# Kernel tuning notes

Hardware: AMD Instinct MI355X
Metric: run time of the kernel (lower is better)

## Reference

```python
import jax, jax.numpy as jnp
import numpy as np

N = 50000   # nodes
E = 800000  # edges (avg degree 16)
IN, HID, OUT = 128, 128, 64


def setup_inputs() -> dict:
    key = jax.random.key(0)
    ks = jax.random.split(key, 8)
    x = jax.random.normal(ks[0], (N, IN), dtype=jnp.float32)
    edge_index = jax.random.randint(ks[1], (2, E), 0, N, dtype=jnp.int32)
    s = 0.05
    W1 = jax.random.normal(ks[2], (IN, HID), dtype=jnp.float32) * s
    b1 = jnp.zeros((HID,), dtype=jnp.float32)
    W2 = jax.random.normal(ks[3], (HID, HID), dtype=jnp.float32) * s
    b2 = jnp.zeros((HID,), dtype=jnp.float32)
    W3 = jax.random.normal(ks[4], (HID, OUT), dtype=jnp.float32) * s
    b3 = jnp.zeros((OUT,), dtype=jnp.float32)
    return {"x": x, "edge_index": edge_index, "W1": W1, "b1": b1,
            "W2": W2, "b2": b2, "W3": W3, "b3": b3}


def _gcn_norm(edge_index, n):
    # PyG GCNConv default: add self-loops, symmetric normalization D^-1/2 A D^-1/2
    loop = jnp.arange(n, dtype=edge_index.dtype)
    src = jnp.concatenate([edge_index[0], loop])  # [E+N]
    dst = jnp.concatenate([edge_index[1], loop])  # [E+N]
    deg = jax.ops.segment_sum(jnp.ones_like(dst, dtype=jnp.float32), dst,
                              num_segments=n)  # degree of destination (col)
    dinv = jax.lax.rsqrt(deg)  # deg >= 1 due to self-loops
    norm = dinv[src] * dinv[dst]  # [E+N]
    return src, dst, norm


def _gcn_conv(x, src, dst, norm, W, b, n):
    h = x @ W                      # [N, F_out]  (transform first, fewer flops)
    msg = h[src] * norm[:, None]   # gather + scale  [E+N, F_out]
    agg = jax.ops.segment_sum(msg, dst, num_segments=n)
    return agg + b


def reference(x, edge_index, W1, b1, W2, b2, W3, b3):
    n = x.shape[0]
    src, dst, norm = _gcn_norm(edge_index, n)
    h = jax.nn.relu(_gcn_conv(x, src, dst, norm, W1, b1, n))
    h = jax.nn.relu(_gcn_conv(h, src, dst, norm, W2, b2, n))
    # dropout p=0.0 / eval mode -> identity
    out = jax.nn.relu(h @ W3 + b3)
    return out
```

## Files before the change

### kernel.cpp

```cpp
#include <hip/hip_runtime.h>
#include <hip/hip_fp16.h>
#include <cstddef>
#include <type_traits>


typedef _Float16 half8 __attribute__((ext_vector_type(8)));
typedef float f32x4 __attribute__((ext_vector_type(4)));

constexpr int CAP = 4608;

__global__ __launch_bounds__(256) void prep(const float* __restrict__ x,
                                            __half* __restrict__ xh, int n4, int ncast,
                                            const float* __restrict__ W1,
                                            const float* __restrict__ W2,
                                            const float* __restrict__ W3,
                                            __half* __restrict__ w1t,
                                            __half* __restrict__ w2t,
                                            __half* __restrict__ w3t,
                                            int* __restrict__ gcount, int nb) {
    int b = blockIdx.x;
    if (b == 0 && threadIdx.x < nb) gcount[threadIdx.x] = 0;
    if (b < ncast) {
        int i = b * 256 + threadIdx.x;
        if (i < n4) {
            float4 v = *(const float4*)&x[(size_t)i * 4];
            __half2 a = __floats2half2_rn(v.x, v.y);
            __half2 c = __floats2half2_rn(v.z, v.w);
            *(int2*)&xh[(size_t)i * 4] = make_int2(*(int*)&a, *(int*)&c);
        }
        return;
    }
    int blk = b - ncast;
    const float* W;
    __half* Wt;
    int ncol, i;
    if (blk < 64) { W = W1; Wt = w1t; ncol = 128; i = blk * 256 + threadIdx.x; }
    else if (blk < 128) { W = W2; Wt = w2t; ncol = 128; i = (blk - 64) * 256 + threadIdx.x; }
    else { W = W3; Wt = w3t; ncol = 64; i = (blk - 128) * 256 + threadIdx.x; }
    if (i < 128 * ncol) {
        int k = i / ncol, c = i - k * ncol;
        Wt[c * 128 + k] = __float2half(W[i]);
    }
}

__global__ __launch_bounds__(1024) void bucket_p1(const int* __restrict__ src,
                                                  const int* __restrict__ dst,
                                                  int* __restrict__ gcount,
                                                  int2* __restrict__ gbucket,
                                                  int nb, int e) {
    __shared__ int lcnt[256];
    __shared__ int lbase[256];
    int t = threadIdx.x;
    if (t < nb) lcnt[t] = 0;
    __syncthreads();

    int base = blockIdx.x * 8192 + t * 8;
    int d[8], s[8], pb[8], pp[8];
    if (base + 8 <= e) {
        *(int4*)&d[0] = *(const int4*)&dst[base];
        *(int4*)&d[4] = *(const int4*)&dst[base + 4];
        *(int4*)&s[0] = *(const int4*)&src[base];
        *(int4*)&s[4] = *(const int4*)&src[base + 4];
    } else {
#pragma unroll
        for (int u = 0; u < 8; ++u) {
            d[u] = (base + u < e) ? dst[base + u] : -1;
            s[u] = (base + u < e) ? src[base + u] : 0;
        }
    }
#pragma unroll
    for (int u = 0; u < 8; ++u) {
        if (d[u] >= 0) {
            pb[u] = d[u] >> 8;
            pp[u] = atomicAdd(&lcnt[pb[u]], 1);
        }
    }
    __syncthreads();
    if (t < nb) lbase[t] = lcnt[t] ? atomicAdd(&gcount[t], lcnt[t]) : 0;
    __syncthreads();
#pragma unroll
    for (int u = 0; u < 8; ++u) {
        if (d[u] >= 0) {
            int p = lbase[pb[u]] + pp[u];
            if (p < CAP) gbucket[(size_t)pb[u] * CAP + p] = make_int2(d[u], s[u]);
        }
    }
}

template <int N, bool EPI, typename OT>
__device__ __forceinline__ void gemm_tile(const __half* __restrict__ Ah,
                                          const __half* __restrict__ Wt,
                                          const float* __restrict__ bias,
                                          OT* __restrict__ C, int M, int tile, int t) {
    constexpr int NC = N / 32;
    const int w = t >> 6, l = t & 63;
    const int lr = l & 15, kg = l >> 4;
    const int rh = w >> 1, ch = w & 1;
    const int r0 = tile * 64 + rh * 32;

    half8 wf[NC][4];
#pragma unroll
    for (int c = 0; c < NC; ++c)
#pragma unroll
        for (int ks = 0; ks < 4; ++ks)
            wf[c][ks] = *(const half8*)&Wt[(size_t)((ch * NC + c) * 16 + lr) * 128 +
                                           ks * 32 + kg * 8];

    f32x4 acc[2][NC];
#pragma unroll
    for (int rt = 0; rt < 2; ++rt)
#pragma unroll
        for (int c = 0; c < NC; ++c) acc[rt][c] = (f32x4){0.f, 0.f, 0.f, 0.f};

    const int row0 = r0 + lr, row1 = r0 + 16 + lr;
    const bool ok0 = row0 < M, ok1 = row1 < M;
#pragma unroll
    for (int ks = 0; ks < 4; ++ks) {
        half8 af0 = (half8)(_Float16)0, af1 = (half8)(_Float16)0;
        if (ok0) af0 = *(const half8*)&Ah[(size_t)row0 * 128 + ks * 32 + kg * 8];
        if (ok1) af1 = *(const half8*)&Ah[(size_t)row1 * 128 + ks * 32 + kg * 8];
#pragma unroll
        for (int c = 0; c < NC; ++c) {
            acc[0][c] = __builtin_amdgcn_mfma_f32_16x16x32_f16(wf[c][ks], af0, acc[0][c], 0, 0, 0);
            acc[1][c] = __builtin_amdgcn_mfma_f32_16x16x32_f16(wf[c][ks], af1, acc[1][c], 0, 0, 0);
        }
    }

#pragma unroll
    for (int rt = 0; rt < 2; ++rt) {
        int row = r0 + rt * 16 + lr;
        if (row < M) {
#pragma unroll
            for (int c = 0; c < NC; ++c) {
                int col = (ch * NC + c) * 16 + kg * 4;
                float v0 = acc[rt][c][0], v1 = acc[rt][c][1];
                float v2 = acc[rt][c][2], v3 = acc[rt][c][3];
                if constexpr (EPI) {
                    float4 bv = *(const float4*)&bias[col];
                    v0 = fmaxf(v0 + bv.x, 0.f);
                    v1 = fmaxf(v1 + bv.y, 0.f);
                    v2 = fmaxf(v2 + bv.z, 0.f);
                    v3 = fmaxf(v3 + bv.w, 0.f);
                }
                if constexpr (std::is_same_v<OT, float>) {
                    *(float4*)&C[(size_t)row * N + col] = make_float4(v0, v1, v2, v3);
                } else {
                    __half2 p0 = __floats2half2_rn(v0, v1);
                    __half2 p1 = __floats2half2_rn(v2, v3);
                    *(int2*)&C[(size_t)row * N + col] = make_int2(*(int*)&p0, *(int*)&p1);
                }
            }
        }
    }
}

__global__ __launch_bounds__(256) void build_and_g1(const int* __restrict__ gcount,
                                                    const int2* __restrict__ gbucket,
                                                    int* __restrict__ offs,
                                                    float* __restrict__ dinv,
                                                    int* __restrict__ eidx,
                                                    const __half* __restrict__ xh,
                                                    const __half* __restrict__ w1t,
                                                    __half* __restrict__ hbuf,
                                                    int n, int nb) {
    __shared__ int srcS[CAP];
    __shared__ int sc[256];
    __shared__ int cur[256];
    const int bid = blockIdx.x, t = threadIdx.x;

    if (bid >= nb) {
        gemm_tile<128, false, __half>(xh, w1t, nullptr, hbuf, n, bid - nb, t);
        return;
    }

    int node0 = bid << 8;
    int own = (t < nb) ? gcount[t] : 0;
    sc[t] = own;
    __syncthreads();
    for (int d = 1; d < 256; d <<= 1) {
        int u = (t >= d) ? sc[t - d] : 0;
        __syncthreads();
        sc[t] += u;
        __syncthreads();
    }
    cur[t] = sc[t] - own;
    if (bid == 0 && t == 0) offs[n] = sc[255];
    __syncthreads();
    int gb = cur[bid];
    int cnt = min(gcount[bid], CAP);
    __syncthreads();

    cur[t] = 0;
    __syncthreads();
    const int2* gbp = gbucket + (size_t)bid * CAP;
    for (int i = t; i < cnt; i += 256) {
        int2 pr = gbp[i];
        atomicAdd(&cur[pr.x - node0], 1);
    }
    __syncthreads();
    own = cur[t];
    sc[t] = own;
    __syncthreads();
    for (int d = 1; d < 256; d <<= 1) {
        int u = (t >= d) ? sc[t - d] : 0;
        __syncthreads();
        sc[t] += u;
        __syncthreads();
    }
    int excl = sc[t] - own;
    int node = node0 + t;
    if (node < n) {
        offs[node] = gb + excl;
        dinv[node] = rsqrtf((float)(own + 1));
    }
    cur[t] = excl;
    __syncthreads();
    for (int i = t; i < cnt; i += 256) {
        int2 pr = gbp[i];
        int pos = atomicAdd(&cur[pr.x - node0], 1);
        srcS[pos] = pr.y;
    }
    __syncthreads();
    for (int i = t; i < cnt; i += 256) eidx[gb + i] = srcS[i];
}

template <int N, bool EPI, typename OT>
__global__ __launch_bounds__(256) void mfma_gemm(const __half* __restrict__ Ah,
                                                 const __half* __restrict__ Wt,
                                                 const float* __restrict__ bias,
                                                 OT* __restrict__ C, int M) {
    gemm_tile<N, EPI, OT>(Ah, Wt, bias, C, M, blockIdx.x, threadIdx.x);
}

__global__ __launch_bounds__(256) void agg_kernel(const __half* __restrict__ h,
                                                  const float* __restrict__ dinv,
                                                  const int* __restrict__ offs,
                                                  const int* __restrict__ eidx,
                                                  const float* __restrict__ bias,
                                                  __half* __restrict__ out, int n) {
    int node = blockIdx.x * 16 + (threadIdx.x >> 4);
    int lane = threadIdx.x & 15;
    if (node >= n) return;
    const int4* h4 = (const int4*)h;
    float dv = dinv[node];

    int4 sp = h4[(size_t)node * 16 + lane];
    float nm = dv * dv;
    float a0, a1, a2, a3, a4, a5, a6, a7;
    {
        float2 f0 = __half22float2(*(__half2*)&sp.x);
        float2 f1 = __half22float2(*(__half2*)&sp.y);
        float2 f2 = __half22float2(*(__half2*)&sp.z);
        float2 f3 = __half22float2(*(__half2*)&sp.w);
        a0 = f0.x * nm; a1 = f0.y * nm; a2 = f1.x * nm; a3 = f1.y * nm;
        a4 = f2.x * nm; a5 = f2.y * nm; a6 = f3.x * nm; a7 = f3.y * nm;
    }

    int beg = offs[node], end = offs[node + 1];
    int j = beg;
    for (; j + 8 <= end; j += 8) {
        int s[8];
        float wg[8];
        int4 hv[8];
#pragma unroll
        for (int u = 0; u < 8; ++u) s[u] = eidx[j + u];
#pragma unroll
        for (int u = 0; u < 8; ++u) {
            wg[u] = dinv[s[u]];
            hv[u] = h4[(size_t)s[u] * 16 + lane];
        }
#pragma unroll
        for (int u = 0; u < 8; ++u) {
            float wu = wg[u] * dv;
            float2 g0 = __half22float2(*(__half2*)&hv[u].x);
            float2 g1 = __half22float2(*(__half2*)&hv[u].y);
            float2 g2 = __half22float2(*(__half2*)&hv[u].z);
            float2 g3 = __half22float2(*(__half2*)&hv[u].w);
            a0 = fmaf(g0.x, wu, a0); a1 = fmaf(g0.y, wu, a1);
            a2 = fmaf(g1.x, wu, a2); a3 = fmaf(g1.y, wu, a3);
            a4 = fmaf(g2.x, wu, a4); a5 = fmaf(g2.y, wu, a5);
            a6 = fmaf(g3.x, wu, a6); a7 = fmaf(g3.y, wu, a7);
        }
    }
    if (j < end) {
        int s[8];
        float wg[8];
        int4 hv[8];
#pragma unroll
        for (int u = 0; u < 8; ++u) {
            int idx = j + u;
            s[u] = eidx[idx < end ? idx : end - 1];
        }
#pragma unroll
        for (int u = 0; u < 8; ++u) {
            wg[u] = (j + u < end) ? dinv[s[u]] : 0.f;
            hv[u] = h4[(size_t)s[u] * 16 + lane];
        }
#pragma unroll
        for (int u = 0; u < 8; ++u) {
            float wu = wg[u] * dv;
            float2 g0 = __half22float2(*(__half2*)&hv[u].x);
            float2 g1 = __half22float2(*(__half2*)&hv[u].y);
            float2 g2 = __half22float2(*(__half2*)&hv[u].z);
            float2 g3 = __half22float2(*(__half2*)&hv[u].w);
            a0 = fmaf(g0.x, wu, a0); a1 = fmaf(g0.y, wu, a1);
            a2 = fmaf(g1.x, wu, a2); a3 = fmaf(g1.y, wu, a3);
            a4 = fmaf(g2.x, wu, a4); a5 = fmaf(g2.y, wu, a5);
            a6 = fmaf(g3.x, wu, a6); a7 = fmaf(g3.y, wu, a7);
        }
    }
    float4 b0 = *(const float4*)&bias[lane * 8];
    float4 b1 = *(const float4*)&bias[lane * 8 + 4];
    a0 = fmaxf(a0 + b0.x, 0.f); a1 = fmaxf(a1 + b0.y, 0.f);
    a2 = fmaxf(a2 + b0.z, 0.f); a3 = fmaxf(a3 + b0.w, 0.f);
    a4 = fmaxf(a4 + b1.x, 0.f); a5 = fmaxf(a5 + b1.y, 0.f);
    a6 = fmaxf(a6 + b1.z, 0.f); a7 = fmaxf(a7 + b1.w, 0.f);
    __half2 o0 = __floats2half2_rn(a0, a1);
    __half2 o1 = __floats2half2_rn(a2, a3);
    __half2 o2 = __floats2half2_rn(a4, a5);
    __half2 o3 = __floats2half2_rn(a6, a7);
    *(int4*)&out[(size_t)node * 128 + lane * 8] =
        make_int4(*(int*)&o0, *(int*)&o1, *(int*)&o2, *(int*)&o3);
}

extern "C" void kernel_launch(void* const* d_in, const int* in_sizes, int n_in,
                              void* d_out, int out_size, void* d_ws, size_t ws_size,
                              hipStream_t stream) {
    const float* x  = (const float*)d_in[0];
    const int* ei   = (const int*)d_in[1];
    const float* W1 = (const float*)d_in[2];
    const float* b1 = (const float*)d_in[3];
    const float* W2 = (const float*)d_in[4];
    const float* b2 = (const float*)d_in[5];
    const float* W3 = (const float*)d_in[6];
    const float* b3 = (const float*)d_in[7];
    float* out = (float*)d_out;

    const int N = in_sizes[0] / 128;
    const int E = in_sizes[1] / 2;
    const int* esrc = ei;
    const int* edst = ei + E;
    const int nb = (N + 255) >> 8;

    char* w = (char*)d_ws;
    size_t off = 0;
    auto alloc = [&](size_t bytes) {
        void* p = w + off;
        off = (off + bytes + 255) & ~(size_t)255;
        return p;
    };
    int*    gcount  = (int*)alloc((size_t)nb * 4);
    int2*   gbucket = (int2*)alloc((size_t)nb * CAP * 8);
    int*    offs    = (int*)alloc((size_t)(N + 1) * 4);
    float*  dinv    = (float*)alloc((size_t)N * 4);
    int*    eidx    = (int*)alloc((size_t)E * 4);
    __half* xh      = (__half*)alloc((size_t)N * 128 * 2);
    __half* w1t     = (__half*)alloc(128 * 128 * 2);
    __half* w2t     = (__half*)alloc(128 * 128 * 2);
    __half* w3t     = (__half*)alloc(64 * 128 * 2);
    __half* hbuf    = (__half*)alloc((size_t)N * 128 * 2);
    __half* abuf    = (__half*)alloc((size_t)N * 128 * 2);
    (void)ws_size;

    const int n4 = N * 32;
    const int ncast = (n4 + 255) / 256;
    const int gemm_blocks = (N + 63) / 64;
    const int agg_blocks = (N + 15) / 16;

    prep<<<ncast + 160, 256, 0, stream>>>(x, xh, n4, ncast, W1, W2, W3,
                                          w1t, w2t, w3t, gcount, nb);
    bucket_p1<<<(E + 8191) / 8192, 1024, 0, stream>>>(esrc, edst, gcount, gbucket, nb, E);
    build_and_g1<<<nb + gemm_blocks, 256, 0, stream>>>(gcount, gbucket, offs, dinv,
                                                       eidx, xh, w1t, hbuf, N, nb);
    agg_kernel<<<agg_blocks, 256, 0, stream>>>(hbuf, dinv, offs, eidx, b1, abuf, N);
    mfma_gemm<128, false, __half><<<gemm_blocks, 256, 0, stream>>>(abuf, w2t, nullptr, hbuf, N);
    agg_kernel<<<agg_blocks, 256, 0, stream>>>(hbuf, dinv, offs, eidx, b2, abuf, N);
    mfma_gemm<64, true, float><<<gemm_blocks, 256, 0, stream>>>(abuf, w3t, b3, out, N);
}
```

Baseline: 132.3 us.

## Fuse aggregation with following GEMM and fold x fp32 cast into first GEMM

The first GEMM now reads x as fp32 and converts it to fp16 in registers, so the separate cast pass and the xh buffer are gone. Each aggregation kernel is fused with the next dense GEMM. The aggregated 16-row tile is staged in XOR-swizzled shared memory and multiplied by W2 or W3 with MFMA in the same block, so the intermediate abuf no longer makes a round trip through HBM. The trade-off is that every 16-node block reloads the full weight fragments from global memory or cache, and the GEMM tiles become smaller.

Result: faster. 116.1 us (-12.3%).

```diff
diff --git a/kernel.cpp b/kernel.cpp
--- a/kernel.cpp
+++ b/kernel.cpp
@@ -9,9 +9,7 @@
 
 constexpr int CAP = 4608;
 
-__global__ __launch_bounds__(256) void prep(const float* __restrict__ x,
-                                            __half* __restrict__ xh, int n4, int ncast,
-                                            const float* __restrict__ W1,
+__global__ __launch_bounds__(256) void prep(const float* __restrict__ W1,
                                             const float* __restrict__ W2,
                                             const float* __restrict__ W3,
                                             __half* __restrict__ w1t,
@@ -20,23 +18,12 @@
                                             int* __restrict__ gcount, int nb) {
     int b = blockIdx.x;
     if (b == 0 && threadIdx.x < nb) gcount[threadIdx.x] = 0;
-    if (b < ncast) {
-        int i = b * 256 + threadIdx.x;
-        if (i < n4) {
-            float4 v = *(const float4*)&x[(size_t)i * 4];
-            __half2 a = __floats2half2_rn(v.x, v.y);
-            __half2 c = __floats2half2_rn(v.z, v.w);
-            *(int2*)&xh[(size_t)i * 4] = make_int2(*(int*)&a, *(int*)&c);
-        }
-        return;
-    }
-    int blk = b - ncast;
     const float* W;
     __half* Wt;
     int ncol, i;
-    if (blk < 64) { W = W1; Wt = w1t; ncol = 128; i = blk * 256 + threadIdx.x; }
-    else if (blk < 128) { W = W2; Wt = w2t; ncol = 128; i = (blk - 64) * 256 + threadIdx.x; }
-    else { W = W3; Wt = w3t; ncol = 64; i = (blk - 128) * 256 + threadIdx.x; }
+    if (b < 64) { W = W1; Wt = w1t; ncol = 128; i = b * 256 + threadIdx.x; }
+    else if (b < 128) { W = W2; Wt = w2t; ncol = 128; i = (b - 64) * 256 + threadIdx.x; }
+    else { W = W3; Wt = w3t; ncol = 64; i = (b - 128) * 256 + threadIdx.x; }
     if (i < 128 * ncol) {
         int k = i / ncol, c = i - k * ncol;
         Wt[c * 128 + k] = __float2half(W[i]);
@@ -87,12 +74,11 @@
     }
 }
 
-template <int N, bool EPI, typename OT>
-__device__ __forceinline__ void gemm_tile(const __half* __restrict__ Ah,
-                                          const __half* __restrict__ Wt,
-                                          const float* __restrict__ bias,
-                                          OT* __restrict__ C, int M, int tile, int t) {
-    constexpr int NC = N / 32;
+__device__ __forceinline__ void gemm_tile_xf32(const float* __restrict__ A,
+                                               const __half* __restrict__ Wt,
+                                               __half* __restrict__ C, int M,
+                                               int tile, int t) {
+    constexpr int NC = 4;
     const int w = t >> 6, l = t & 63;
     const int lr = l & 15, kg = l >> 4;
     const int rh = w >> 1, ch = w & 1;
@@ -117,8 +103,22 @@
 #pragma unroll
     for (int ks = 0; ks < 4; ++ks) {
         half8 af0 = (half8)(_Float16)0, af1 = (half8)(_Float16)0;
-        if (ok0) af0 = *(const half8*)&Ah[(size_t)row0 * 128 + ks * 32 + kg * 8];
-        if (ok1) af1 = *(const half8*)&Ah[(size_t)row1 * 128 + ks * 32 + kg * 8];
+        if (ok0) {
+            float4 p = *(const float4*)&A[(size_t)row0 * 128 + ks * 32 + kg * 8];
+            float4 q = *(const float4*)&A[(size_t)row0 * 128 + ks * 32 + kg * 8 + 4];
+            af0[0] = (_Float16)p.x; af0[1] = (_Float16)p.y;
+            af0[2] = (_Float16)p.z; af0[3] = (_Float16)p.w;
+            af0[4] = (_Float16)q.x; af0[5] = (_Float16)q.y;
+            af0[6] = (_Float16)q.z; af0[7] = (_Float16)q.w;
+        }
+        if (ok1) {
+            float4 p = *(const float4*)&A[(size_t)row1 * 128 + ks * 32 + kg * 8];
+            float4 q = *(const float4*)&A[(size_t)row1 * 128 + ks * 32 + kg * 8 + 4];
+            af1[0] = (_Float16)p.x; af1[1] = (_Float16)p.y;
+            af1[2] = (_Float16)p.z; af1[3] = (_Float16)p.w;
+            af1[4] = (_Float16)q.x; af1[5] = (_Float16)q.y;
+            af1[6] = (_Float16)q.z; af1[7] = (_Float16)q.w;
+        }
 #pragma unroll
         for (int c = 0; c < NC; ++c) {
             acc[0][c] = __builtin_amdgcn_mfma_f32_16x16x32_f16(wf[c][ks], af0, acc[0][c], 0, 0, 0);
@@ -133,22 +133,9 @@
 #pragma unroll
             for (int c = 0; c < NC; ++c) {
                 int col = (ch * NC + c) * 16 + kg * 4;
-                float v0 = acc[rt][c][0], v1 = acc[rt][c][1];
-                float v2 = acc[rt][c][2], v3 = acc[rt][c][3];
-                if constexpr (EPI) {
-                    float4 bv = *(const float4*)&bias[col];
-                    v0 = fmaxf(v0 + bv.x, 0.f);
-                    v1 = fmaxf(v1 + bv.y, 0.f);
-                    v2 = fmaxf(v2 + bv.z, 0.f);
-                    v3 = fmaxf(v3 + bv.w, 0.f);
-                }
-                if constexpr (std::is_same_v<OT, float>) {
-                    *(float4*)&C[(size_t)row * N + col] = make_float4(v0, v1, v2, v3);
-                } else {
-                    __half2 p0 = __floats2half2_rn(v0, v1);
-                    __half2 p1 = __floats2half2_rn(v2, v3);
-                    *(int2*)&C[(size_t)row * N + col] = make_int2(*(int*)&p0, *(int*)&p1);
-                }
+                __half2 p0 = __floats2half2_rn(acc[rt][c][0], acc[rt][c][1]);
+                __half2 p1 = __floats2half2_rn(acc[rt][c][2], acc[rt][c][3]);
+                *(int2*)&C[(size_t)row * 128 + col] = make_int2(*(int*)&p0, *(int*)&p1);
             }
         }
     }
@@ -159,9 +146,9 @@
                                                     int* __restrict__ offs,
                                                     float* __restrict__ dinv,
                                                     int* __restrict__ eidx,
-                                                    const __half* __restrict__ xh,
+                                                    const float* __restrict__ x,
                                                     const __half* __restrict__ w1t,
-                                                    __half* __restrict__ hbuf,
+                                                    __half* __restrict__ g1buf,
                                                     int n, int nb) {
     __shared__ int srcS[CAP];
     __shared__ int sc[256];
@@ -169,7 +156,7 @@
     const int bid = blockIdx.x, t = threadIdx.x;
 
     if (bid >= nb) {
-        gemm_tile<128, false, __half>(xh, w1t, nullptr, hbuf, n, bid - nb, t);
+        gemm_tile_xf32(x, w1t, g1buf, n, bid - nb, t);
         return;
     }
 
@@ -224,103 +211,160 @@
     for (int i = t; i < cnt; i += 256) eidx[gb + i] = srcS[i];
 }
 
-template <int N, bool EPI, typename OT>
-__global__ __launch_bounds__(256) void mfma_gemm(const __half* __restrict__ Ah,
-                                                 const __half* __restrict__ Wt,
-                                                 const float* __restrict__ bias,
-                                                 OT* __restrict__ C, int M) {
-    gemm_tile<N, EPI, OT>(Ah, Wt, bias, C, M, blockIdx.x, threadIdx.x);
-}
-
-__global__ __launch_bounds__(256) void agg_kernel(const __half* __restrict__ h,
-                                                  const float* __restrict__ dinv,
-                                                  const int* __restrict__ offs,
-                                                  const int* __restrict__ eidx,
-                                                  const float* __restrict__ bias,
-                                                  __half* __restrict__ out, int n) {
-    int node = blockIdx.x * 16 + (threadIdx.x >> 4);
-    int lane = threadIdx.x & 15;
-    if (node >= n) return;
-    const int4* h4 = (const int4*)h;
-    float dv = dinv[node];
-
-    int4 sp = h4[(size_t)node * 16 + lane];
-    float nm = dv * dv;
-    float a0, a1, a2, a3, a4, a5, a6, a7;
+template <int N2, bool EPI, typename OT>
+__global__ __launch_bounds__(256) void agg_gemm(const __half* __restrict__ g,
+                                                const float* __restrict__ dinv,
+                                                const int* __restrict__ offs,
+                                                const int* __restrict__ eidx,
+                                                const float* __restrict__ biasA,
+                                                const __half* __restrict__ Wt,
+                                                const float* __restrict__ biasG,
+                                                OT* __restrict__ C, int n) {
+    __shared__ alignas(16) char hs[16 * 256];
+    const int t = threadIdx.x;
+    const int node0 = blockIdx.x * 16;
+
     {
-        float2 f0 = __half22float2(*(__half2*)&sp.x);
-        float2 f1 = __half22float2(*(__half2*)&sp.y);
-        float2 f2 = __half22float2(*(__half2*)&sp.z);
-        float2 f3 = __half22float2(*(__half2*)&sp.w);
-        a0 = f0.x * nm; a1 = f0.y * nm; a2 = f1.x * nm; a3 = f1.y * nm;
-        a4 = f2.x * nm; a5 = f2.y * nm; a6 = f3.x * nm; a7 = f3.y * nm;
-    }
-
-    int beg = offs[node], end = offs[node + 1];
-    int j = beg;
-    for (; j + 8 <= end; j += 8) {
-        int s[8];
-        float wg[8];
-        int4 hv[8];
-#pragma unroll
-        for (int u = 0; u < 8; ++u) s[u] = eidx[j + u];
-#pragma unroll
-        for (int u = 0; u < 8; ++u) {
-            wg[u] = dinv[s[u]];
-            hv[u] = h4[(size_t)s[u] * 16 + lane];
-        }
-#pragma unroll
-        for (int u = 0; u < 8; ++u) {
-            float wu = wg[u] * dv;
-            float2 g0 = __half22float2(*(__half2*)&hv[u].x);
-            float2 g1 = __half22float2(*(__half2*)&hv[u].y);
-            float2 g2 = __half22float2(*(__half2*)&hv[u].z);
-            float2 g3 = __half22float2(*(__half2*)&hv[u].w);
-            a0 = fmaf(g0.x, wu, a0); a1 = fmaf(g0.y, wu, a1);
-            a2 = fmaf(g1.x, wu, a2); a3 = fmaf(g1.y, wu, a3);
-            a4 = fmaf(g2.x, wu, a4); a5 = fmaf(g2.y, wu, a5);
-            a6 = fmaf(g3.x, wu, a6); a7 = fmaf(g3.y, wu, a7);
-        }
-    }
-    if (j < end) {
-        int s[8];
-        float wg[8];
-        int4 hv[8];
-#pragma unroll
-        for (int u = 0; u < 8; ++u) {
-            int idx = j + u;
-            s[u] = eidx[idx < end ? idx : end - 1];
-        }
-#pragma unroll
-        for (int u = 0; u < 8; ++u) {
-            wg[u] = (j + u < end) ? dinv[s[u]] : 0.f;
-            hv[u] = h4[(size_t)s[u] * 16 + lane];
-        }
-#pragma unroll
-        for (int u = 0; u < 8; ++u) {
-            float wu = wg[u] * dv;
-            float2 g0 = __half22float2(*(__half2*)&hv[u].x);
-            float2 g1 = __half22float2(*(__half2*)&hv[u].y);
-            float2 g2 = __half22float2(*(__half2*)&hv[u].z);
-            float2 g3 = __half22float2(*(__half2*)&hv[u].w);
-            a0 = fmaf(g0.x, wu, a0); a1 = fmaf(g0.y, wu, a1);
-            a2 = fmaf(g1.x, wu, a2); a3 = fmaf(g1.y, wu, a3);
-            a4 = fmaf(g2.x, wu, a4); a5 = fmaf(g2.y, wu, a5);
-            a6 = fmaf(g3.x, wu, a6); a7 = fmaf(g3.y, wu, a7);
-        }
-    }
-    float4 b0 = *(const float4*)&bias[lane * 8];
-    float4 b1 = *(const float4*)&bias[lane * 8 + 4];
-    a0 = fmaxf(a0 + b0.x, 0.f); a1 = fmaxf(a1 + b0.y, 0.f);
-    a2 = fmaxf(a2 + b0.z, 0.f); a3 = fmaxf(a3 + b0.w, 0.f);
-    a4 = fmaxf(a4 + b1.x, 0.f); a5 = fmaxf(a5 + b1.y, 0.f);
-    a6 = fmaxf(a6 + b1.z, 0.f); a7 = fmaxf(a7 + b1.w, 0.f);
-    __half2 o0 = __floats2half2_rn(a0, a1);
-    __half2 o1 = __floats2half2_rn(a2, a3);
-    __half2 o2 = __floats2half2_rn(a4, a5);
-    __half2 o3 = __floats2half2_rn(a6, a7);
-    *(int4*)&out[(size_t)node * 128 + lane * 8] =
-        make_int4(*(int*)&o0, *(int*)&o1, *(int*)&o2, *(int*)&o3);
+        int row = t >> 4;
+        int lane = t & 15;
+        int node = node0 + row;
+        int bo = (lane * 16) ^ ((row & 7) << 4);
+        if (node < n) {
+            const int4* h4 = (const int4*)g;
+            float dv = dinv[node];
+            int4 sp = h4[(size_t)node * 16 + lane];
+            float nm = dv * dv;
+            float a0, a1, a2, a3, a4, a5, a6, a7;
+            {
+                float2 f0 = __half22float2(*(__half2*)&sp.x);
+                float2 f1 = __half22float2(*(__half2*)&sp.y);
+                float2 f2 = __half22float2(*(__half2*)&sp.z);
+                float2 f3 = __half22float2(*(__half2*)&sp.w);
+                a0 = f0.x * nm; a1 = f0.y * nm; a2 = f1.x * nm; a3 = f1.y * nm;
+                a4 = f2.x * nm; a5 = f2.y * nm; a6 = f3.x * nm; a7 = f3.y * nm;
+            }
+            int beg = offs[node], end = offs[node + 1];
+            int j = beg;
+            for (; j + 8 <= end; j += 8) {
+                int s[8];
+                float wg[8];
+                int4 hv[8];
+#pragma unroll
+                for (int u = 0; u < 8; ++u) s[u] = eidx[j + u];
+#pragma unroll
+                for (int u = 0; u < 8; ++u) {
+                    wg[u] = dinv[s[u]];
+                    hv[u] = h4[(size_t)s[u] * 16 + lane];
+                }
+#pragma unroll
+                for (int u = 0; u < 8; ++u) {
+                    float wu = wg[u] * dv;
+                    float2 g0 = __half22float2(*(__half2*)&hv[u].x);
+                    float2 g1 = __half22float2(*(__half2*)&hv[u].y);
+                    float2 g2 = __half22float2(*(__half2*)&hv[u].z);
+                    float2 g3 = __half22float2(*(__half2*)&hv[u].w);
+                    a0 = fmaf(g0.x, wu, a0); a1 = fmaf(g0.y, wu, a1);
+                    a2 = fmaf(g1.x, wu, a2); a3 = fmaf(g1.y, wu, a3);
+                    a4 = fmaf(g2.x, wu, a4); a5 = fmaf(g2.y, wu, a5);
+                    a6 = fmaf(g3.x, wu, a6); a7 = fmaf(g3.y, wu, a7);
+                }
+            }
+            if (j < end) {
+                int s[8];
+                float wg[8];
+                int4 hv[8];
+#pragma unroll
+                for (int u = 0; u < 8; ++u) {
+                    int idx = j + u;
+                    s[u] = eidx[idx < end ? idx : end - 1];
+                }
+#pragma unroll
+                for (int u = 0; u < 8; ++u) {
+                    wg[u] = (j + u < end) ? dinv[s[u]] : 0.f;
+                    hv[u] = h4[(size_t)s[u] * 16 + lane];
+                }
+#pragma unroll
+                for (int u = 0; u < 8; ++u) {
+                    float wu = wg[u] * dv;
+                    float2 g0 = __half22float2(*(__half2*)&hv[u].x);
+                    float2 g1 = __half22float2(*(__half2*)&hv[u].y);
+                    float2 g2 = __half22float2(*(__half2*)&hv[u].z);
+                    float2 g3 = __half22float2(*(__half2*)&hv[u].w);
+                    a0 = fmaf(g0.x, wu, a0); a1 = fmaf(g0.y, wu, a1);
+                    a2 = fmaf(g1.x, wu, a2); a3 = fmaf(g1.y, wu, a3);
+                    a4 = fmaf(g2.x, wu, a4); a5 = fmaf(g2.y, wu, a5);
+                    a6 = fmaf(g3.x, wu, a6); a7 = fmaf(g3.y, wu, a7);
+                }
+            }
+            float4 b0 = *(const float4*)&biasA[lane * 8];
+            float4 b1 = *(const float4*)&biasA[lane * 8 + 4];
+            a0 = fmaxf(a0 + b0.x, 0.f); a1 = fmaxf(a1 + b0.y, 0.f);
+            a2 = fmaxf(a2 + b0.z, 0.f); a3 = fmaxf(a3 + b0.w, 0.f);
+            a4 = fmaxf(a4 + b1.x, 0.f); a5 = fmaxf(a5 + b1.y, 0.f);
+            a6 = fmaxf(a6 + b1.z, 0.f); a7 = fmaxf(a7 + b1.w, 0.f);
+            __half2 o0 = __floats2half2_rn(a0, a1);
+            __half2 o1 = __floats2half2_rn(a2, a3);
+            __half2 o2 = __floats2half2_rn(a4, a5);
+            __half2 o3 = __floats2half2_rn(a6, a7);
+            *(int4*)&hs[row * 256 + bo] =
+                make_int4(*(int*)&o0, *(int*)&o1, *(int*)&o2, *(int*)&o3);
+        } else {
+            *(int4*)&hs[row * 256 + bo] = make_int4(0, 0, 0, 0);
+        }
+    }
+    __syncthreads();
+
+    constexpr int NW = N2 / 4;
+    constexpr int NC = NW / 16;
+    const int w = t >> 6, l = t & 63;
+    const int lr = l & 15, kg = l >> 4;
+
+    half8 wf[NC][4];
+#pragma unroll
+    for (int c = 0; c < NC; ++c)
+#pragma unroll
+        for (int ks = 0; ks < 4; ++ks)
+            wf[c][ks] = *(const half8*)&Wt[(size_t)(w * NW + c * 16 + lr) * 128 +
+                                           ks * 32 + kg * 8];
+
+    half8 af[4];
+#pragma unroll
+    for (int ks = 0; ks < 4; ++ks) {
+        int bo = (ks * 64 + kg * 16) ^ ((lr & 7) << 4);
+        af[ks] = *(const half8*)&hs[lr * 256 + bo];
+    }
+
+    f32x4 acc[NC];
+#pragma unroll
+    for (int c = 0; c < NC; ++c) acc[c] = (f32x4){0.f, 0.f, 0.f, 0.f};
+#pragma unroll
+    for (int ks = 0; ks < 4; ++ks)
+#pragma unroll
+        for (int c = 0; c < NC; ++c)
+            acc[c] = __builtin_amdgcn_mfma_f32_16x16x32_f16(wf[c][ks], af[ks], acc[c], 0, 0, 0);
+
+    int row = node0 + lr;
+    if (row < n) {
+#pragma unroll
+        for (int c = 0; c < NC; ++c) {
+            int col = w * NW + c * 16 + kg * 4;
+            float v0 = acc[c][0], v1 = acc[c][1], v2 = acc[c][2], v3 = acc[c][3];
+            if constexpr (EPI) {
+                float4 bv = *(const float4*)&biasG[col];
+                v0 = fmaxf(v0 + bv.x, 0.f);
+                v1 = fmaxf(v1 + bv.y, 0.f);
+                v2 = fmaxf(v2 + bv.z, 0.f);
+                v3 = fmaxf(v3 + bv.w, 0.f);
+            }
+            if constexpr (std::is_same_v<OT, float>) {
+                *(float4*)&C[(size_t)row * N2 + col] = make_float4(v0, v1, v2, v3);
+            } else {
+                __half2 p0 = __floats2half2_rn(v0, v1);
+                __half2 p1 = __floats2half2_rn(v2, v3);
+                *(int2*)&C[(size_t)row * N2 + col] = make_int2(*(int*)&p0, *(int*)&p1);
+            }
+        }
+    }
 }
 
 extern "C" void kernel_launch(void* const* d_in, const int* in_sizes, int n_in,
@@ -354,26 +398,22 @@
     int*    offs    = (int*)alloc((size_t)(N + 1) * 4);
     float*  dinv    = (float*)alloc((size_t)N * 4);
     int*    eidx    = (int*)alloc((size_t)E * 4);
-    __half* xh      = (__half*)alloc((size_t)N * 128 * 2);
     __half* w1t     = (__half*)alloc(128 * 128 * 2);
     __half* w2t     = (__half*)alloc(128 * 128 * 2);
     __half* w3t     = (__half*)alloc(64 * 128 * 2);
-    __half* hbuf    = (__half*)alloc((size_t)N * 128 * 2);
-    __half* abuf    = (__half*)alloc((size_t)N * 128 * 2);
+    __half* g1buf   = (__half*)alloc((size_t)N * 128 * 2);
+    __half* g2buf   = (__half*)alloc((size_t)N * 128 * 2);
     (void)ws_size;
 
-    const int n4 = N * 32;
-    const int ncast = (n4 + 255) / 256;
     const int gemm_blocks = (N + 63) / 64;
     const int agg_blocks = (N + 15) / 16;
 
-    prep<<<ncast + 160, 256, 0, stream>>>(x, xh, n4, ncast, W1, W2, W3,
-                                          w1t, w2t, w3t, gcount, nb);
+    prep<<<160, 256, 0, stream>>>(W1, W2, W3, w1t, w2t, w3t, gcount, nb);
     bucket_p1<<<(E + 8191) / 8192, 1024, 0, stream>>>(esrc, edst, gcount, gbucket, nb, E);
     build_and_g1<<<nb + gemm_blocks, 256, 0, stream>>>(gcount, gbucket, offs, dinv,
-                                                       eidx, xh, w1t, hbuf, N, nb);
-    agg_kernel<<<agg_blocks, 256, 0, stream>>>(hbuf, dinv, offs, eidx, b1, abuf, N);
-    mfma_gemm<128, false, __half><<<gemm_blocks, 256, 0, stream>>>(abuf, w2t, nullptr, hbuf, N);
-    agg_kernel<<<agg_blocks, 256, 0, stream>>>(hbuf, dinv, offs, eidx, b2, abuf, N);
-    mfma_gemm<64, true, float><<<gemm_blocks, 256, 0, stream>>>(abuf, w3t, b3, out, N);
-}
+                                                       eidx, x, w1t, g1buf, N, nb);
+    agg_gemm<128, false, __half><<<agg_blocks, 256, 0, stream>>>(
+        g1buf, dinv, offs, eidx, b1, w2t, nullptr, g2buf, N);
+    agg_gemm<64, true, float><<<agg_blocks, 256, 0, stream>>>(
+        g2buf, dinv, offs, eidx, b2, w3t, b3, out, N);
+}
```
